# Optimization experiments

Hardware: AMD Instinct MI355X
Metric: run time of the kernel (lower is better)

Reference implementation:

```python
import jax, jax.numpy as jnp
import numpy as np

NUM_HEADS = 12
TOP_P = 0.9


def setup_inputs() -> dict:
    key = jax.random.key(0)
    ks = jax.random.split(key, 5)
    B, N, C = 2, 2048, 768
    return {
        "x": jax.random.normal(ks[0], (B, N, C), jnp.float32),
        "qkv_w": jax.random.normal(ks[1], (3 * C, C), jnp.float32) * (C ** -0.5),
        "proj_w": jax.random.normal(ks[2], (C, C), jnp.float32) * (C ** -0.5),
        "proj_b": jax.random.normal(ks[3], (C,), jnp.float32) * 0.02,
        "temperature": jnp.ones((1,), jnp.float32),
        "top_k": 64,
    }


def reference(x, qkv_w, proj_w, proj_b, temperature, top_k):
    B, N, C = x.shape
    H = NUM_HEADS
    D = C // H
    # qkv projection: [B,N,3C] -> [3,B,H,N,D]
    qkv = (x @ qkv_w.T).reshape(B, N, 3, H, D).transpose(2, 0, 3, 1, 4)
    q, k, v = qkv[0], qkv[1], qkv[2]
    scale = (D ** -0.5) * temperature  # (1,) broadcasts
    attn = jnp.einsum("bhnd,bhmd->bhnm", q, k) * scale  # [B,H,N,N]
    neg_inf = jnp.asarray(-jnp.inf, attn.dtype)
    # top-k filtering: keep only scores >= k-th largest per row
    kth = jax.lax.top_k(attn, top_k)[0][..., -1:]
    attn = jnp.where(attn < kth, neg_inf, attn)
    # top-p (nucleus) filtering on sorted scores
    order = jnp.argsort(-attn, axis=-1)  # descending sort indices
    sorted_attn = jnp.take_along_axis(attn, order, axis=-1)
    cum = jnp.cumsum(jax.nn.softmax(sorted_attn, axis=-1), axis=-1)
    rm = cum > TOP_P
    # shift right by one, always keep the top entry
    rm = jnp.concatenate([jnp.zeros_like(rm[..., :1]), rm[..., :-1]], axis=-1)
    # scatter back to original positions via inverse permutation
    inv = jnp.argsort(order, axis=-1)
    remove = jnp.take_along_axis(rm, inv, axis=-1)
    attn = jnp.where(remove, neg_inf, attn)
    p = jax.nn.softmax(attn, axis=-1)
    out = jnp.einsum("bhnm,bhmd->bhnd", p, v)  # [B,H,N,D]
    out = out.transpose(0, 2, 1, 3).reshape(B, N, C)
    return out @ proj_w.T + proj_b
```

## Files before the change

### kernel.cpp

```cpp
#include <hip/hip_runtime.h>
#include <cstdint>

#define NH 12
#define HD 64
#define NSEQ 2048
#define CDIM 768
#define NB 2

typedef __attribute__((ext_vector_type(2))) float f32x2;

__global__ __launch_bounds__(256, 4) void qkv_qk(const float* __restrict__ x,
                                                 const float* __restrict__ w,
                                                 double* __restrict__ Q64,
                                                 double* __restrict__ K64,
                                                 float* __restrict__ Qs32,
                                                 float* __restrict__ Kt32) {
    __shared__ double As[16][128];
    __shared__ double Bs[16][64];
    const int tid = threadIdx.x;
    const int bm = blockIdx.y * 128;
    const int bn = blockIdx.x * 64;
    const int alm = tid >> 1, alk = (tid & 1) * 8;
    const int blm = tid & 63, blk = (tid >> 6) * 4;
    const int tx = tid & 15, ty = tid >> 4;

    double acc[8][4] = {};
    float4 a0 = *reinterpret_cast<const float4*>(&x[(bm + alm) * CDIM + alk]);
    float4 a1 = *reinterpret_cast<const float4*>(&x[(bm + alm) * CDIM + alk + 4]);
    float4 b0 = *reinterpret_cast<const float4*>(&w[(bn + blm) * CDIM + blk]);
    for (int k0 = 0; k0 < CDIM; k0 += 16) {
        __syncthreads();
        As[alk + 0][alm] = (double)a0.x; As[alk + 1][alm] = (double)a0.y;
        As[alk + 2][alm] = (double)a0.z; As[alk + 3][alm] = (double)a0.w;
        As[alk + 4][alm] = (double)a1.x; As[alk + 5][alm] = (double)a1.y;
        As[alk + 6][alm] = (double)a1.z; As[alk + 7][alm] = (double)a1.w;
        Bs[blk + 0][blm] = (double)b0.x; Bs[blk + 1][blm] = (double)b0.y;
        Bs[blk + 2][blm] = (double)b0.z; Bs[blk + 3][blm] = (double)b0.w;
        __syncthreads();
        if (k0 + 16 < CDIM) {
            a0 = *reinterpret_cast<const float4*>(&x[(bm + alm) * CDIM + k0 + 16 + alk]);
            a1 = *reinterpret_cast<const float4*>(&x[(bm + alm) * CDIM + k0 + 16 + alk + 4]);
            b0 = *reinterpret_cast<const float4*>(&w[(bn + blm) * CDIM + k0 + 16 + blk]);
        }
#pragma unroll
        for (int k = 0; k < 16; ++k) {
            double ad[8], bd[4];
#pragma unroll
            for (int i = 0; i < 8; ++i) ad[i] = As[k][ty * 8 + i];
#pragma unroll
            for (int j = 0; j < 4; ++j) bd[j] = Bs[k][tx * 4 + j];
#pragma unroll
            for (int i = 0; i < 8; ++i)
#pragma unroll
                for (int j = 0; j < 4; ++j) acc[i][j] = fma(ad[i], bd[j], acc[i][j]);
        }
    }
    const bool isQ = bn < CDIM;
    const int hh = (isQ ? bn : bn - CDIM) >> 6;
    const int b  = bm >> 11;
    const int bh = b * NH + hh;
#pragma unroll
    for (int i = 0; i < 8; ++i) {
        const int n = (bm + ty * 8 + i) & (NSEQ - 1);
        const size_t base = ((size_t)bh * NSEQ + n) * HD + tx * 4;
        if (isQ) {
            double2 d01; d01.x = acc[i][0]; d01.y = acc[i][1];
            double2 d23; d23.x = acc[i][2]; d23.y = acc[i][3];
            *reinterpret_cast<double2*>(&Q64[base]) = d01;
            *reinterpret_cast<double2*>(&Q64[base + 2]) = d23;
            *reinterpret_cast<float4*>(&Qs32[base]) =
                make_float4((float)acc[i][0], (float)acc[i][1], (float)acc[i][2], (float)acc[i][3]);
        } else {
            double2 d01; d01.x = acc[i][0]; d01.y = acc[i][1];
            double2 d23; d23.x = acc[i][2]; d23.y = acc[i][3];
            *reinterpret_cast<double2*>(&K64[base]) = d01;
            *reinterpret_cast<double2*>(&K64[base + 2]) = d23;
#pragma unroll
            for (int j = 0; j < 4; ++j)
                Kt32[((size_t)bh * HD + tx * 4 + j) * NSEQ + n] = (float)acc[i][j];
        }
    }
}

__global__ __launch_bounds__(256) void qkv_v(const float* __restrict__ x,
                                             const float* __restrict__ wv,
                                             float* __restrict__ V) {
    __shared__ float As[16][64];
    __shared__ float Bs[16][64];
    const int tid = threadIdx.x;
    const int bm = blockIdx.y * 64;
    const int bn = blockIdx.x * 64;
    const int lm = tid >> 2;
    const int lk = (tid & 3) << 2;
    const int tx = tid & 15, ty = tid >> 4;

    float acc[4][4] = {};
    float4 av = *reinterpret_cast<const float4*>(&x[(bm + lm) * CDIM + lk]);
    float4 bv = *reinterpret_cast<const float4*>(&wv[(bn + lm) * CDIM + lk]);
    for (int k0 = 0; k0 < CDIM; k0 += 16) {
        __syncthreads();
        As[lk + 0][lm] = av.x; As[lk + 1][lm] = av.y; As[lk + 2][lm] = av.z; As[lk + 3][lm] = av.w;
        Bs[lk + 0][lm] = bv.x; Bs[lk + 1][lm] = bv.y; Bs[lk + 2][lm] = bv.z; Bs[lk + 3][lm] = bv.w;
        __syncthreads();
        if (k0 + 16 < CDIM) {
            av = *reinterpret_cast<const float4*>(&x[(bm + lm) * CDIM + k0 + 16 + lk]);
            bv = *reinterpret_cast<const float4*>(&wv[(bn + lm) * CDIM + k0 + 16 + lk]);
        }
#pragma unroll
        for (int k = 0; k < 16; ++k) {
            float4 a4 = *reinterpret_cast<const float4*>(&As[k][ty * 4]);
            float4 b4 = *reinterpret_cast<const float4*>(&Bs[k][tx * 4]);
            float aa[4] = {a4.x, a4.y, a4.z, a4.w};
            float bb[4] = {b4.x, b4.y, b4.z, b4.w};
#pragma unroll
            for (int i = 0; i < 4; ++i)
#pragma unroll
                for (int j = 0; j < 4; ++j) acc[i][j] = fmaf(aa[i], bb[j], acc[i][j]);
        }
    }
    const int hh = bn >> 6;
    const int b  = bm >> 11;
#pragma unroll
    for (int i = 0; i < 4; ++i) {
        const int n = (bm + ty * 4 + i) & (NSEQ - 1);
        *reinterpret_cast<float4*>(&V[(((size_t)b * NH + hh) * NSEQ + n) * HD + tx * 4]) =
            make_float4(acc[i][0], acc[i][1], acc[i][2], acc[i][3]);
    }
}

__device__ inline unsigned long long d2key(double f) {
    unsigned long long u = (unsigned long long)__double_as_longlong(f);
    return u ^ (unsigned long long)(((long long)u >> 63) | (long long)0x8000000000000000ull);
}
__device__ inline double key2d(unsigned long long k) {
    unsigned long long mask = ((long long)k < 0) ? 0x8000000000000000ull : 0xFFFFFFFFFFFFFFFFull;
    return __longlong_as_double((long long)(k ^ mask));
}
__device__ inline unsigned kp(float a, float b) {
    unsigned ua = __float_as_uint(a);
    ua ^= (unsigned)(((int)ua >> 31) | 0x80000000);
    unsigned ub = __float_as_uint(b);
    ub ^= (unsigned)(((int)ub >> 31) | 0x80000000);
    return (ua >> 16) | (ub & 0xFFFF0000u);
}

__global__ __launch_bounds__(512, 6) void attn_kernel(const double* __restrict__ Q64,
                                                      const double* __restrict__ K64,
                                                      const float* __restrict__ Qs32,
                                                      const float* __restrict__ Kt32,
                                                      const float* __restrict__ V,
                                                      const float* __restrict__ temp,
                                                      const int* __restrict__ topk_p,
                                                      float* __restrict__ AO) {
    __shared__ unsigned short sk[8][NSEQ];
    __shared__ int cand[8][128];

    const int tid  = threadIdx.x;
    const int wg   = (blockIdx.x & 7) * 768 + (blockIdx.x >> 3);
    const int bh   = wg >> 8;
    const int g0   = (wg & 255) << 3;
    const int lane = tid & 63;
    const int wv   = tid >> 6;

    const double scale = 0.125 * (double)temp[0];
    const float sc32 = (float)scale;
    int TK = *topk_p;
    if (TK > 64) TK = 64;
    if (TK < 1)  TK = 1;

    const float* __restrict__ kb = Kt32 + (size_t)bh * HD * NSEQ;
    const float* __restrict__ qp = Qs32 + ((size_t)bh * NSEQ + g0) * HD;
    const int m0 = tid * 4;
    f32x2 acc2[8][2] = {};
#pragma unroll 4
    for (int d = 0; d < HD; ++d) {
        float4 k4 = *reinterpret_cast<const float4*>(&kb[(size_t)d * NSEQ + m0]);
        f32x2 kA; kA.x = k4.x; kA.y = k4.y;
        f32x2 kB; kB.x = k4.z; kB.y = k4.w;
#pragma unroll
        for (int r8 = 0; r8 < 8; ++r8) {
            float qv = qp[r8 * HD + d];
            f32x2 qq; qq.x = qv; qq.y = qv;
            acc2[r8][0] = __builtin_elementwise_fma(qq, kA, acc2[r8][0]);
            acc2[r8][1] = __builtin_elementwise_fma(qq, kB, acc2[r8][1]);
        }
    }
#pragma unroll
    for (int r8 = 0; r8 < 8; ++r8) {
        uint2 pkv;
        pkv.x = kp(acc2[r8][0].x * sc32, acc2[r8][0].y * sc32);
        pkv.y = kp(acc2[r8][1].x * sc32, acc2[r8][1].y * sc32);
        *reinterpret_cast<uint2*>(&sk[r8][m0]) = pkv;
    }
    __syncthreads();

    const int r = wv;
    const int row = g0 + r;

    int k32[32];
#pragma unroll
    for (int i = 0; i < 32; ++i) k32[i] = sk[r][i * 64 + lane];

    int mx = k32[0];
#pragma unroll
    for (int i = 1; i < 32; ++i) mx = max(mx, k32[i]);
#pragma unroll
    for (int off = 32; off > 0; off >>= 1) mx = max(mx, __shfl_xor(mx, off));

    int lo0 = mx > 512 ? mx - 512 : 0;
    int c0 = 0;
#pragma unroll
    for (int i = 0; i < 32; ++i) c0 += (int)__popcll(__ballot(k32[i] >= lo0));
    int lo, hi, clo;
    if (c0 >= TK) { lo = lo0; clo = c0; hi = mx; }
    else          { lo = 0;   clo = NSEQ; hi = lo0 - 1; }
    while (lo < hi && clo > 72) {
        int mid = lo + ((hi - lo + 1) >> 1);
        int c = 0;
#pragma unroll
        for (int i = 0; i < 32; ++i) c += (int)__popcll(__ballot(k32[i] >= mid));
        if (c >= TK) { lo = mid; clo = c; } else hi = mid - 1;
    }
    int thr = lo >= 2 ? lo - 2 : 0;

    const unsigned long long lmask = (1ull << lane) - 1ull;
    int base = 0;
#pragma unroll
    for (int i = 0; i < 32; ++i) {
        bool pred = k32[i] >= thr;
        unsigned long long bal = __ballot(pred);
        if (pred) {
            int slot = base + (int)__popcll(bal & lmask);
            if (slot < 128) cand[r][slot] = i * 64 + lane;
        }
        base += (int)__popcll(bal);
    }
    int ncand = min(base, 128);
    asm volatile("s_waitcnt lgkmcnt(0)" ::: "memory");

    const int gidx = lane >> 3;
    const int sl   = lane & 7;
    const double* __restrict__ qrow = Q64 + ((size_t)bh * NSEQ + row) * HD;
    double qd[8];
#pragma unroll
    for (int j = 0; j < 8; ++j) qd[j] = qrow[sl * 8 + j];

    int msArr[16];
#pragma unroll
    for (int j = 0; j < 16; ++j) msArr[j] = cand[r][min(j * 8 + gidx, ncand - 1)];

    unsigned long long* pkr = reinterpret_cast<unsigned long long*>(&sk[r][0]);
    pkr[lane] = 0ull;
    pkr[64 + lane] = 0ull;
    const double* __restrict__ kbase = K64 + (size_t)bh * NSEQ * HD;
    const int jmax = (ncand + 7) >> 3;
#pragma unroll 2
    for (int j = 0; j < jmax; ++j) {
        const int s = j * 8 + gidx;
        const int ms = msArr[j];
        const double* __restrict__ kp8 = kbase + (size_t)ms * HD + sl * 8;
        double a = 0.0;
#pragma unroll
        for (int d = 0; d < 8; ++d) a = fma(qd[d], kp8[d], a);
        a += __shfl_xor(a, 1);
        a += __shfl_xor(a, 2);
        a += __shfl_xor(a, 4);
        a *= scale;
        unsigned long long pkv = (d2key(a) & ~2047ull) | (unsigned long long)(2047 - ms);
        if (sl == (j & 7) && s < ncand) pkr[s] = pkv;
    }
    asm volatile("s_waitcnt lgkmcnt(0)" ::: "memory");
    unsigned long long pk1 = pkr[lane];
    unsigned long long pk2 = pkr[64 + lane];

    unsigned long long t0 = ~pk1, t1 = ~pk2;
#pragma unroll
    for (int k = 2; k <= 64; k <<= 1) {
#pragma unroll
        for (int j = k >> 1; j > 0; j >>= 1) {
            {
                unsigned long long ot = __shfl_xor(t0, j);
                bool dir = (lane & k) != 0;
                bool lower = (lane & j) == 0;
                bool takeMin = (lower != dir);
                bool less = t0 < ot;
                t0 = (takeMin == less) ? t0 : ot;
            }
            {
                unsigned long long ot = __shfl_xor(t1, j);
                bool dir = (k == 64) ? true : ((lane & k) != 0);
                bool lower = (lane & j) == 0;
                bool takeMin = (lower != dir);
                bool less = t1 < ot;
                t1 = (takeMin == less) ? t1 : ot;
            }
        }
    }
    {
        unsigned long long na = (t1 < t0) ? t1 : t0;
        unsigned long long nb = (t1 < t0) ? t0 : t1;
        t0 = na; t1 = nb;
    }
#pragma unroll
    for (int j = 32; j > 0; j >>= 1) {
        {
            unsigned long long ot = __shfl_xor(t0, j);
            bool lower = (lane & j) == 0;
            bool less = t0 < ot;
            t0 = (lower == less) ? t0 : ot;
        }
        {
            unsigned long long ot = __shfl_xor(t1, j);
            bool lower = (lane & j) == 0;
            bool less = t1 < ot;
            t1 = (lower == less) ? t1 : ot;
        }
    }
    unsigned long long kk = ~t0;
    int mi = 2047 - (int)(kk & 2047ull);
    bool valid = lane < TK;
    double a = valid ? key2d(kk & ~2047ull) : 0.0;
    double amax = __shfl(a, 0);
    double s = valid ? exp(a - amax) : 0.0;

    double ps = s;
#pragma unroll
    for (int off = 1; off < 64; off <<= 1) {
        double tt = __shfl_up(ps, off);
        if (lane >= off) ps += tt;
    }
    double S = __shfl(ps, 63);
    double cumprev = (ps - s) / S;
    bool keep = valid && ((lane == 0) || (cumprev <= 0.9));
    double sk2 = keep ? s : 0.0;
    double S2 = sk2;
#pragma unroll
    for (int off = 32; off > 0; off >>= 1) S2 += __shfl_xor(S2, off);
    float p = (float)(keep ? (s / S2) : 0.0);

    unsigned long long bal = __ballot(keep);
    int nk = __popcll(bal);

    const float* __restrict__ vb = V + (size_t)bh * NSEQ * HD;
    float o = 0.f;
    for (int i = 0; i < nk; ++i) {
        float pi = __shfl(p, i);
        int midx = __shfl(mi, i);
        o = fmaf(pi, vb[(size_t)midx * HD + lane], o);
    }
    const int b = bh / NH, hh = bh % NH;
    AO[((size_t)b * NSEQ + row) * CDIM + hh * HD + lane] = o;
}

__global__ __launch_bounds__(256) void proj_gemm(const float* __restrict__ A,
                                                 const float* __restrict__ w,
                                                 const float* __restrict__ bias,
                                                 float* __restrict__ out) {
    __shared__ float As[16][128];
    __shared__ float Bs[16][64];
    const int tid = threadIdx.x;
    const int bm = blockIdx.y * 128;
    const int bn = blockIdx.x * 64;
    const int alm = tid >> 1, alk = (tid & 1) * 8;
    const int blm = tid & 63, blk = (tid >> 6) * 4;
    const int tx = tid & 15, ty = tid >> 4;

    float acc[8][4] = {};
    float4 a0 = *reinterpret_cast<const float4*>(&A[(bm + alm) * CDIM + alk]);
    float4 a1 = *reinterpret_cast<const float4*>(&A[(bm + alm) * CDIM + alk + 4]);
    float4 b0 = *reinterpret_cast<const float4*>(&w[(bn + blm) * CDIM + blk]);
    for (int k0 = 0; k0 < CDIM; k0 += 16) {
        __syncthreads();
        As[alk + 0][alm] = a0.x; As[alk + 1][alm] = a0.y;
        As[alk + 2][alm] = a0.z; As[alk + 3][alm] = a0.w;
        As[alk + 4][alm] = a1.x; As[alk + 5][alm] = a1.y;
        As[alk + 6][alm] = a1.z; As[alk + 7][alm] = a1.w;
        Bs[blk + 0][blm] = b0.x; Bs[blk + 1][blm] = b0.y;
        Bs[blk + 2][blm] = b0.z; Bs[blk + 3][blm] = b0.w;
        __syncthreads();
        if (k0 + 16 < CDIM) {
            a0 = *reinterpret_cast<const float4*>(&A[(bm + alm) * CDIM + k0 + 16 + alk]);
            a1 = *reinterpret_cast<const float4*>(&A[(bm + alm) * CDIM + k0 + 16 + alk + 4]);
            b0 = *reinterpret_cast<const float4*>(&w[(bn + blm) * CDIM + k0 + 16 + blk]);
        }
#pragma unroll
        for (int k = 0; k < 16; ++k) {
            float4 af0 = *reinterpret_cast<const float4*>(&As[k][ty * 8]);
            float4 af1 = *reinterpret_cast<const float4*>(&As[k][ty * 8 + 4]);
            float4 bf  = *reinterpret_cast<const float4*>(&Bs[k][tx * 4]);
            float aa[8] = {af0.x, af0.y, af0.z, af0.w, af1.x, af1.y, af1.z, af1.w};
            float bb[4] = {bf.x, bf.y, bf.z, bf.w};
#pragma unroll
            for (int i = 0; i < 8; ++i)
#pragma unroll
                for (int j = 0; j < 4; ++j) acc[i][j] = fmaf(aa[i], bb[j], acc[i][j]);
        }
    }
    float4 bv = *reinterpret_cast<const float4*>(&bias[bn + tx * 4]);
#pragma unroll
    for (int i = 0; i < 8; ++i) {
        int rr = bm + ty * 8 + i;
        float4 v4 = make_float4(acc[i][0] + bv.x, acc[i][1] + bv.y,
                                acc[i][2] + bv.z, acc[i][3] + bv.w);
        *reinterpret_cast<float4*>(&out[(size_t)rr * CDIM + bn + tx * 4]) = v4;
    }
}

extern "C" void kernel_launch(void* const* d_in, const int* in_sizes, int n_in,
                              void* d_out, int out_size, void* d_ws, size_t ws_size,
                              hipStream_t stream) {
    const float* x      = (const float*)d_in[0];
    const float* qkv_w  = (const float*)d_in[1];
    const float* proj_w = (const float*)d_in[2];
    const float* proj_b = (const float*)d_in[3];
    const float* temp   = (const float*)d_in[4];
    const int*   topk   = (const int*)d_in[5];
    float* out = (float*)d_out;

    const size_t HSZ = (size_t)NB * NH * NSEQ * HD;
    double* Q64  = (double*)d_ws;
    double* K64  = Q64 + HSZ;
    float*  Qs32 = (float*)(K64 + HSZ);
    float*  Kt32 = Qs32 + HSZ;
    float*  V    = Kt32 + HSZ;
    float*  AO   = V + HSZ;

    qkv_qk<<<dim3(24, 32), 256, 0, stream>>>(x, qkv_w, Q64, K64, Qs32, Kt32);
    qkv_v<<<dim3(12, 64), 256, 0, stream>>>(x, qkv_w + (size_t)2 * CDIM * CDIM, V);
    attn_kernel<<<dim3(NB * NH * (NSEQ / 8)), 512, 0, stream>>>(Q64, K64, Qs32, Kt32, V, temp, topk, AO);
    proj_gemm<<<dim3(12, 32), 256, 0, stream>>>(AO, proj_w, proj_b, out);
}
```

Measured before the change: 713.1 us.

## Fuse QK and V projection kernels, vectorize LDS loads, trim final merge, unroll gather

Merges the double-precision Q/K projection and the fp32 V projection into one launch, with blocks branching on blockIdx and sharing one raw shared-memory buffer. The Q/K inner loop now reads shared memory as double2 vectors. In the attention kernel, the final bitonic merge tracks only the lower half it needs instead of both halves. The V-gather loop is unrolled by four with independent accumulators to expose more memory-level parallelism. The intent is to remove one launch and let both GEMMs run concurrently, cut LDS and shuffle instructions, and hide gather latency. The fused kernel uses the larger shared-memory footprint and the 256,4 launch bounds for the V blocks too, and the reordered fp32 sums change rounding slightly.

Result: faster. 669.7 us (median of 3 runs) (-6.1%).

```diff
diff --git a/kernel.cpp b/kernel.cpp
--- a/kernel.cpp
+++ b/kernel.cpp
@@ -9,122 +9,125 @@
 
 typedef __attribute__((ext_vector_type(2))) float f32x2;
 
-__global__ __launch_bounds__(256, 4) void qkv_qk(const float* __restrict__ x,
-                                                 const float* __restrict__ w,
-                                                 double* __restrict__ Q64,
-                                                 double* __restrict__ K64,
-                                                 float* __restrict__ Qs32,
-                                                 float* __restrict__ Kt32) {
-    __shared__ double As[16][128];
-    __shared__ double Bs[16][64];
+__global__ __launch_bounds__(256, 4) void qkv_fused(const float* __restrict__ x,
+                                                    const float* __restrict__ w,
+                                                    double* __restrict__ Q64,
+                                                    double* __restrict__ K64,
+                                                    float* __restrict__ Qs32,
+                                                    float* __restrict__ Kt32,
+                                                    float* __restrict__ V) {
+    __shared__ __align__(16) char smem[24576];
     const int tid = threadIdx.x;
-    const int bm = blockIdx.y * 128;
-    const int bn = blockIdx.x * 64;
-    const int alm = tid >> 1, alk = (tid & 1) * 8;
-    const int blm = tid & 63, blk = (tid >> 6) * 4;
-    const int tx = tid & 15, ty = tid >> 4;
-
-    double acc[8][4] = {};
-    float4 a0 = *reinterpret_cast<const float4*>(&x[(bm + alm) * CDIM + alk]);
-    float4 a1 = *reinterpret_cast<const float4*>(&x[(bm + alm) * CDIM + alk + 4]);
-    float4 b0 = *reinterpret_cast<const float4*>(&w[(bn + blm) * CDIM + blk]);
-    for (int k0 = 0; k0 < CDIM; k0 += 16) {
-        __syncthreads();
-        As[alk + 0][alm] = (double)a0.x; As[alk + 1][alm] = (double)a0.y;
-        As[alk + 2][alm] = (double)a0.z; As[alk + 3][alm] = (double)a0.w;
-        As[alk + 4][alm] = (double)a1.x; As[alk + 5][alm] = (double)a1.y;
-        As[alk + 6][alm] = (double)a1.z; As[alk + 7][alm] = (double)a1.w;
-        Bs[blk + 0][blm] = (double)b0.x; Bs[blk + 1][blm] = (double)b0.y;
-        Bs[blk + 2][blm] = (double)b0.z; Bs[blk + 3][blm] = (double)b0.w;
-        __syncthreads();
-        if (k0 + 16 < CDIM) {
-            a0 = *reinterpret_cast<const float4*>(&x[(bm + alm) * CDIM + k0 + 16 + alk]);
-            a1 = *reinterpret_cast<const float4*>(&x[(bm + alm) * CDIM + k0 + 16 + alk + 4]);
-            b0 = *reinterpret_cast<const float4*>(&w[(bn + blm) * CDIM + k0 + 16 + blk]);
-        }
-#pragma unroll
-        for (int k = 0; k < 16; ++k) {
-            double ad[8], bd[4];
-#pragma unroll
-            for (int i = 0; i < 8; ++i) ad[i] = As[k][ty * 8 + i];
-#pragma unroll
-            for (int j = 0; j < 4; ++j) bd[j] = Bs[k][tx * 4 + j];
-#pragma unroll
-            for (int i = 0; i < 8; ++i)
-#pragma unroll
-                for (int j = 0; j < 4; ++j) acc[i][j] = fma(ad[i], bd[j], acc[i][j]);
-        }
-    }
-    const bool isQ = bn < CDIM;
-    const int hh = (isQ ? bn : bn - CDIM) >> 6;
-    const int b  = bm >> 11;
-    const int bh = b * NH + hh;
-#pragma unroll
-    for (int i = 0; i < 8; ++i) {
-        const int n = (bm + ty * 8 + i) & (NSEQ - 1);
-        const size_t base = ((size_t)bh * NSEQ + n) * HD + tx * 4;
-        if (isQ) {
+
+    if (blockIdx.x < 768) {
+        double (*As)[128] = reinterpret_cast<double(*)[128]>(smem);
+        double (*Bs)[64]  = reinterpret_cast<double(*)[64]>(smem + 16384);
+        const int bm = (blockIdx.x / 24) * 128;
+        const int bn = (blockIdx.x % 24) * 64;
+        const int alm = tid >> 1, alk = (tid & 1) * 8;
+        const int blm = tid & 63, blk = (tid >> 6) * 4;
+        const int tx = tid & 15, ty = tid >> 4;
+
+        double acc[8][4] = {};
+        float4 a0 = *reinterpret_cast<const float4*>(&x[(bm + alm) * CDIM + alk]);
+        float4 a1 = *reinterpret_cast<const float4*>(&x[(bm + alm) * CDIM + alk + 4]);
+        float4 b0 = *reinterpret_cast<const float4*>(&w[(bn + blm) * CDIM + blk]);
+        for (int k0 = 0; k0 < CDIM; k0 += 16) {
+            __syncthreads();
+            As[alk + 0][alm] = (double)a0.x; As[alk + 1][alm] = (double)a0.y;
+            As[alk + 2][alm] = (double)a0.z; As[alk + 3][alm] = (double)a0.w;
+            As[alk + 4][alm] = (double)a1.x; As[alk + 5][alm] = (double)a1.y;
+            As[alk + 6][alm] = (double)a1.z; As[alk + 7][alm] = (double)a1.w;
+            Bs[blk + 0][blm] = (double)b0.x; Bs[blk + 1][blm] = (double)b0.y;
+            Bs[blk + 2][blm] = (double)b0.z; Bs[blk + 3][blm] = (double)b0.w;
+            __syncthreads();
+            if (k0 + 16 < CDIM) {
+                a0 = *reinterpret_cast<const float4*>(&x[(bm + alm) * CDIM + k0 + 16 + alk]);
+                a1 = *reinterpret_cast<const float4*>(&x[(bm + alm) * CDIM + k0 + 16 + alk + 4]);
+                b0 = *reinterpret_cast<const float4*>(&w[(bn + blm) * CDIM + k0 + 16 + blk]);
+            }
+#pragma unroll
+            for (int k = 0; k < 16; ++k) {
+                double2 a01 = *reinterpret_cast<const double2*>(&As[k][ty * 8 + 0]);
+                double2 a23 = *reinterpret_cast<const double2*>(&As[k][ty * 8 + 2]);
+                double2 a45 = *reinterpret_cast<const double2*>(&As[k][ty * 8 + 4]);
+                double2 a67 = *reinterpret_cast<const double2*>(&As[k][ty * 8 + 6]);
+                double2 b01 = *reinterpret_cast<const double2*>(&Bs[k][tx * 4 + 0]);
+                double2 b23 = *reinterpret_cast<const double2*>(&Bs[k][tx * 4 + 2]);
+                double ad[8] = {a01.x, a01.y, a23.x, a23.y, a45.x, a45.y, a67.x, a67.y};
+                double bd[4] = {b01.x, b01.y, b23.x, b23.y};
+#pragma unroll
+                for (int i = 0; i < 8; ++i)
+#pragma unroll
+                    for (int j = 0; j < 4; ++j) acc[i][j] = fma(ad[i], bd[j], acc[i][j]);
+            }
+        }
+        const bool isQ = bn < CDIM;
+        const int hh = (isQ ? bn : bn - CDIM) >> 6;
+        const int b  = bm >> 11;
+        const int bh = b * NH + hh;
+#pragma unroll
+        for (int i = 0; i < 8; ++i) {
+            const int n = (bm + ty * 8 + i) & (NSEQ - 1);
+            const size_t base = ((size_t)bh * NSEQ + n) * HD + tx * 4;
             double2 d01; d01.x = acc[i][0]; d01.y = acc[i][1];
             double2 d23; d23.x = acc[i][2]; d23.y = acc[i][3];
-            *reinterpret_cast<double2*>(&Q64[base]) = d01;
-            *reinterpret_cast<double2*>(&Q64[base + 2]) = d23;
-            *reinterpret_cast<float4*>(&Qs32[base]) =
-                make_float4((float)acc[i][0], (float)acc[i][1], (float)acc[i][2], (float)acc[i][3]);
-        } else {
-            double2 d01; d01.x = acc[i][0]; d01.y = acc[i][1];
-            double2 d23; d23.x = acc[i][2]; d23.y = acc[i][3];
-            *reinterpret_cast<double2*>(&K64[base]) = d01;
-            *reinterpret_cast<double2*>(&K64[base + 2]) = d23;
-#pragma unroll
-            for (int j = 0; j < 4; ++j)
-                Kt32[((size_t)bh * HD + tx * 4 + j) * NSEQ + n] = (float)acc[i][j];
-        }
-    }
-}
-
-__global__ __launch_bounds__(256) void qkv_v(const float* __restrict__ x,
-                                             const float* __restrict__ wv,
-                                             float* __restrict__ V) {
-    __shared__ float As[16][64];
-    __shared__ float Bs[16][64];
-    const int tid = threadIdx.x;
-    const int bm = blockIdx.y * 64;
-    const int bn = blockIdx.x * 64;
-    const int lm = tid >> 2;
-    const int lk = (tid & 3) << 2;
-    const int tx = tid & 15, ty = tid >> 4;
-
-    float acc[4][4] = {};
-    float4 av = *reinterpret_cast<const float4*>(&x[(bm + lm) * CDIM + lk]);
-    float4 bv = *reinterpret_cast<const float4*>(&wv[(bn + lm) * CDIM + lk]);
-    for (int k0 = 0; k0 < CDIM; k0 += 16) {
-        __syncthreads();
-        As[lk + 0][lm] = av.x; As[lk + 1][lm] = av.y; As[lk + 2][lm] = av.z; As[lk + 3][lm] = av.w;
-        Bs[lk + 0][lm] = bv.x; Bs[lk + 1][lm] = bv.y; Bs[lk + 2][lm] = bv.z; Bs[lk + 3][lm] = bv.w;
-        __syncthreads();
-        if (k0 + 16 < CDIM) {
-            av = *reinterpret_cast<const float4*>(&x[(bm + lm) * CDIM + k0 + 16 + lk]);
-            bv = *reinterpret_cast<const float4*>(&wv[(bn + lm) * CDIM + k0 + 16 + lk]);
-        }
-#pragma unroll
-        for (int k = 0; k < 16; ++k) {
-            float4 a4 = *reinterpret_cast<const float4*>(&As[k][ty * 4]);
-            float4 b4 = *reinterpret_cast<const float4*>(&Bs[k][tx * 4]);
-            float aa[4] = {a4.x, a4.y, a4.z, a4.w};
-            float bb[4] = {b4.x, b4.y, b4.z, b4.w};
-#pragma unroll
-            for (int i = 0; i < 4; ++i)
-#pragma unroll
-                for (int j = 0; j < 4; ++j) acc[i][j] = fmaf(aa[i], bb[j], acc[i][j]);
-        }
-    }
-    const int hh = bn >> 6;
-    const int b  = bm >> 11;
-#pragma unroll
-    for (int i = 0; i < 4; ++i) {
-        const int n = (bm + ty * 4 + i) & (NSEQ - 1);
-        *reinterpret_cast<float4*>(&V[(((size_t)b * NH + hh) * NSEQ + n) * HD + tx * 4]) =
-            make_float4(acc[i][0], acc[i][1], acc[i][2], acc[i][3]);
+            if (isQ) {
+                *reinterpret_cast<double2*>(&Q64[base]) = d01;
+                *reinterpret_cast<double2*>(&Q64[base + 2]) = d23;
+                *reinterpret_cast<float4*>(&Qs32[base]) =
+                    make_float4((float)acc[i][0], (float)acc[i][1], (float)acc[i][2], (float)acc[i][3]);
+            } else {
+                *reinterpret_cast<double2*>(&K64[base]) = d01;
+                *reinterpret_cast<double2*>(&K64[base + 2]) = d23;
+#pragma unroll
+                for (int j = 0; j < 4; ++j)
+                    Kt32[((size_t)bh * HD + tx * 4 + j) * NSEQ + n] = (float)acc[i][j];
+            }
+        }
+    } else {
+        float (*As)[64] = reinterpret_cast<float(*)[64]>(smem);
+        float (*Bs)[64] = reinterpret_cast<float(*)[64]>(smem + 4096);
+        const float* __restrict__ wv = w + (size_t)2 * CDIM * CDIM;
+        const int vid = blockIdx.x - 768;
+        const int bm = (vid / 12) * 64;
+        const int bn = (vid % 12) * 64;
+        const int lm = tid >> 2;
+        const int lk = (tid & 3) << 2;
+        const int tx = tid & 15, ty = tid >> 4;
+
+        float acc[4][4] = {};
+        float4 av = *reinterpret_cast<const float4*>(&x[(bm + lm) * CDIM + lk]);
+        float4 bv = *reinterpret_cast<const float4*>(&wv[(bn + lm) * CDIM + lk]);
+        for (int k0 = 0; k0 < CDIM; k0 += 16) {
+            __syncthreads();
+            As[lk + 0][lm] = av.x; As[lk + 1][lm] = av.y; As[lk + 2][lm] = av.z; As[lk + 3][lm] = av.w;
+            Bs[lk + 0][lm] = bv.x; Bs[lk + 1][lm] = bv.y; Bs[lk + 2][lm] = bv.z; Bs[lk + 3][lm] = bv.w;
+            __syncthreads();
+            if (k0 + 16 < CDIM) {
+                av = *reinterpret_cast<const float4*>(&x[(bm + lm) * CDIM + k0 + 16 + lk]);
+                bv = *reinterpret_cast<const float4*>(&wv[(bn + lm) * CDIM + k0 + 16 + lk]);
+            }
+#pragma unroll
+            for (int k = 0; k < 16; ++k) {
+                float4 a4 = *reinterpret_cast<const float4*>(&As[k][ty * 4]);
+                float4 b4 = *reinterpret_cast<const float4*>(&Bs[k][tx * 4]);
+                float aa[4] = {a4.x, a4.y, a4.z, a4.w};
+                float bb[4] = {b4.x, b4.y, b4.z, b4.w};
+#pragma unroll
+                for (int i = 0; i < 4; ++i)
+#pragma unroll
+                    for (int j = 0; j < 4; ++j) acc[i][j] = fmaf(aa[i], bb[j], acc[i][j]);
+            }
+        }
+        const int hh = bn >> 6;
+        const int b  = bm >> 11;
+#pragma unroll
+        for (int i = 0; i < 4; ++i) {
+            const int n = (bm + ty * 4 + i) & (NSEQ - 1);
+            *reinterpret_cast<float4*>(&V[(((size_t)b * NH + hh) * NSEQ + n) * HD + tx * 4]) =
+                make_float4(acc[i][0], acc[i][1], acc[i][2], acc[i][3]);
+        }
     }
 }
 
@@ -296,25 +299,13 @@
             }
         }
     }
-    {
-        unsigned long long na = (t1 < t0) ? t1 : t0;
-        unsigned long long nb = (t1 < t0) ? t0 : t1;
-        t0 = na; t1 = nb;
-    }
+    t0 = (t1 < t0) ? t1 : t0;
 #pragma unroll
     for (int j = 32; j > 0; j >>= 1) {
-        {
-            unsigned long long ot = __shfl_xor(t0, j);
-            bool lower = (lane & j) == 0;
-            bool less = t0 < ot;
-            t0 = (lower == less) ? t0 : ot;
-        }
-        {
-            unsigned long long ot = __shfl_xor(t1, j);
-            bool lower = (lane & j) == 0;
-            bool less = t1 < ot;
-            t1 = (lower == less) ? t1 : ot;
-        }
+        unsigned long long ot = __shfl_xor(t0, j);
+        bool lower = (lane & j) == 0;
+        bool less = t0 < ot;
+        t0 = (lower == less) ? t0 : ot;
     }
     unsigned long long kk = ~t0;
     int mi = 2047 - (int)(kk & 2047ull);
@@ -342,12 +333,24 @@
     int nk = __popcll(bal);
 
     const float* __restrict__ vb = V + (size_t)bh * NSEQ * HD;
-    float o = 0.f;
-    for (int i = 0; i < nk; ++i) {
+    float o0 = 0.f, o1 = 0.f, o2 = 0.f, o3 = 0.f;
+    int i = 0;
+    for (; i + 4 <= nk; i += 4) {
+        float pa = __shfl(p, i),     pb = __shfl(p, i + 1);
+        float pc = __shfl(p, i + 2), pd = __shfl(p, i + 3);
+        int ma = __shfl(mi, i),     mb2 = __shfl(mi, i + 1);
+        int mc = __shfl(mi, i + 2), md = __shfl(mi, i + 3);
+        o0 = fmaf(pa, vb[(size_t)ma * HD + lane], o0);
+        o1 = fmaf(pb, vb[(size_t)mb2 * HD + lane], o1);
+        o2 = fmaf(pc, vb[(size_t)mc * HD + lane], o2);
+        o3 = fmaf(pd, vb[(size_t)md * HD + lane], o3);
+    }
+    for (; i < nk; ++i) {
         float pi = __shfl(p, i);
         int midx = __shfl(mi, i);
-        o = fmaf(pi, vb[(size_t)midx * HD + lane], o);
-    }
+        o0 = fmaf(pi, vb[(size_t)midx * HD + lane], o0);
+    }
+    float o = (o0 + o1) + (o2 + o3);
     const int b = bh / NH, hh = bh % NH;
     AO[((size_t)b * NSEQ + row) * CDIM + hh * HD + lane] = o;
 }
@@ -425,8 +428,7 @@
     float*  V    = Kt32 + HSZ;
     float*  AO   = V + HSZ;
 
-    qkv_qk<<<dim3(24, 32), 256, 0, stream>>>(x, qkv_w, Q64, K64, Qs32, Kt32);
-    qkv_v<<<dim3(12, 64), 256, 0, stream>>>(x, qkv_w + (size_t)2 * CDIM * CDIM, V);
+    qkv_fused<<<dim3(1536), 256, 0, stream>>>(x, qkv_w, Q64, K64, Qs32, Kt32, V);
     attn_kernel<<<dim3(NB * NH * (NSEQ / 8)), 512, 0, stream>>>(Q64, K64, Qs32, Kt32, V, temp, topk, AO);
     proj_gemm<<<dim3(12, 32), 256, 0, stream>>>(AO, proj_w, proj_b, out);
 }
```
